# Performance work log

Measured on AMD Instinct MI355X. Metric: run time of the kernel, lower is better.

Reference implementation:

```python
import jax, jax.numpy as jnp
import numpy as np

B, S, D, H, FF = 4, 2048, 512, 8, 2048
HD = D // H
WINDOW = 64  # local attention half-window in rank space
EPS = 1e-5


def _layer_norm(v, g, b):
    m = jnp.mean(v, axis=-1, keepdims=True)
    var = jnp.mean(jnp.square(v - m), axis=-1, keepdims=True)
    return (v - m) / jnp.sqrt(var + EPS) * g + b


def setup_inputs() -> dict:
    key = jax.random.key(0)
    ks = jax.random.split(key, 10)
    sc = 0.02
    x = jax.random.normal(ks[0], (B, S, D), jnp.float32)
    padding_mask = jnp.zeros((B, S), dtype=bool)
    i = jnp.arange(S)
    local = jnp.abs(i[:, None] - i[None, :]) <= WINDOW
    glob = (i[:, None] == 0) | (i[None, :] == 0)  # global spectrum token at pos 0
    attn_mask = jnp.where(local | glob, 0.0, -jnp.inf).astype(jnp.float32)
    return {
        "x": x,
        "padding_mask": padding_mask,
        "attn_mask": attn_mask,
        "in_proj_w": jax.random.normal(ks[1], (3 * D, D), jnp.float32) * sc,
        "in_proj_b": jnp.zeros((3 * D,), jnp.float32),
        "out_proj_w": jax.random.normal(ks[2], (D, D), jnp.float32) * sc,
        "out_proj_b": jnp.zeros((D,), jnp.float32),
        "ln1_g": jnp.ones((D,), jnp.float32),
        "ln1_b": jnp.zeros((D,), jnp.float32),
        "ln2_g": jnp.ones((D,), jnp.float32),
        "ln2_b": jnp.zeros((D,), jnp.float32),
        "ff_w1": jax.random.normal(ks[3], (FF, D), jnp.float32) * sc,
        "ff_b1": jnp.zeros((FF,), jnp.float32),
        "ff_w2": jax.random.normal(ks[4], (D, FF), jnp.float32) * sc,
        "ff_b2": jnp.zeros((D,), jnp.float32),
    }


def reference(x, padding_mask, attn_mask, in_proj_w, in_proj_b, out_proj_w,
              out_proj_b, ln1_g, ln1_b, ln2_g, ln2_b, ff_w1, ff_b1, ff_w2, ff_b2):
    # pre-LN attention
    a = _layer_norm(x, ln1_g, ln1_b)
    qkv = a @ in_proj_w.T + in_proj_b  # [B,S,3D]
    q, k, v = jnp.split(qkv, 3, axis=-1)
    to_heads = lambda t: t.reshape(B, S, H, HD).transpose(0, 2, 1, 3)
    q, k, v = to_heads(q), to_heads(k), to_heads(v)
    scores = jnp.einsum('bhqd,bhkd->bhqk', q, k) * (HD ** -0.5)
    # float attn_mask path: key_padding_mask converted to additive -inf floats
    kpm = jnp.where(padding_mask, -jnp.inf, 0.0).astype(scores.dtype)
    scores = scores + attn_mask[None, None, :, :] + kpm[:, None, None, :]
    p = jax.nn.softmax(scores, axis=-1)
    o = jnp.einsum('bhqk,bhkd->bhqd', p, v).transpose(0, 2, 1, 3).reshape(B, S, D)
    o = o @ out_proj_w.T + out_proj_b
    x = x + o  # residual (dropout = 0)
    # pre-LN feed-forward with exact GELU (torch nn.GELU default)
    f = _layer_norm(x, ln2_g, ln2_b)
    f = jax.nn.gelu(f @ ff_w1.T + ff_b1, approximate=False) @ ff_w2.T + ff_b2
    return x + f
```

## Files before the change

### kernel.cpp

```cpp
#include <hip/hip_runtime.h>
#include <hip/hip_bf16.h>
#include <math.h>

namespace {

constexpr int kB = 4, kS = 2048, kD = 512, kH = 8, kFF = 2048;
constexpr int kM = kB * kS;
constexpr int kHD = kD / kH;
constexpr int kWin = 64;

typedef __attribute__((ext_vector_type(8))) short short8;
typedef __attribute__((ext_vector_type(4))) float f32x4;

__device__ __forceinline__ float bf2f(__hip_bfloat16 v) { return __bfloat162float(v); }
__device__ __forceinline__ __hip_bfloat16 f2bf(float v) { return __float2bfloat16(v); }
__device__ __forceinline__ int iclamp(int v, int lo, int hi) { return v < lo ? lo : (v > hi ? hi : v); }

__device__ __forceinline__ void async16(const void* g, void* l) {
  __builtin_amdgcn_global_load_lds((const __attribute__((address_space(1))) void*)g,
                                   (__attribute__((address_space(3))) void*)l, 16, 0, 0);
}

__global__ void cast_f32_bf16(const float* __restrict__ s, __hip_bfloat16* __restrict__ d, int n) {
  int i = (blockIdx.x * blockDim.x + threadIdx.x) * 4;
  if (i >= n) return;
  float4 v = *(const float4*)(s + i);
  union { __hip_bfloat16 h[4]; uint2 u; } t;
  t.h[0] = f2bf(v.x); t.h[1] = f2bf(v.y); t.h[2] = f2bf(v.z); t.h[3] = f2bf(v.w);
  *(uint2*)(d + i) = t.u;
}

__global__ __launch_bounds__(64)
void ln_rows(const float* __restrict__ x, const float* __restrict__ g,
             const float* __restrict__ bta, __hip_bfloat16* __restrict__ out) {
  int row = blockIdx.x;
  int lane = threadIdx.x;
  const float* xr = x + (size_t)row * kD;
  int c = lane * 8;
  float4 v0 = *(const float4*)(xr + c);
  float4 v1 = *(const float4*)(xr + c + 4);
  float s  = v0.x + v0.y + v0.z + v0.w + v1.x + v1.y + v1.z + v1.w;
  float ss = v0.x*v0.x + v0.y*v0.y + v0.z*v0.z + v0.w*v0.w
           + v1.x*v1.x + v1.y*v1.y + v1.z*v1.z + v1.w*v1.w;
#pragma unroll
  for (int o = 32; o > 0; o >>= 1) { s += __shfl_xor(s, o); ss += __shfl_xor(ss, o); }
  float mean = s * (1.0f / kD);
  float inv  = rsqrtf(ss * (1.0f / kD) - mean * mean + 1e-5f);
  float4 g0 = *(const float4*)(g + c),   g1 = *(const float4*)(g + c + 4);
  float4 b0 = *(const float4*)(bta + c), b1 = *(const float4*)(bta + c + 4);
  union { __hip_bfloat16 h[8]; int4 u; } t;
  t.h[0] = f2bf((v0.x - mean) * inv * g0.x + b0.x);
  t.h[1] = f2bf((v0.y - mean) * inv * g0.y + b0.y);
  t.h[2] = f2bf((v0.z - mean) * inv * g0.z + b0.z);
  t.h[3] = f2bf((v0.w - mean) * inv * g0.w + b0.w);
  t.h[4] = f2bf((v1.x - mean) * inv * g1.x + b1.x);
  t.h[5] = f2bf((v1.y - mean) * inv * g1.y + b1.y);
  t.h[6] = f2bf((v1.z - mean) * inv * g1.z + b1.z);
  t.h[7] = f2bf((v1.w - mean) * inv * g1.w + b1.w);
  *(int4*)(out + (size_t)row * kD + c) = t.u;
}

__global__ __launch_bounds__(64)
void transpose_v(const __hip_bfloat16* __restrict__ qkv, __hip_bfloat16* __restrict__ vt) {
  const int id = blockIdx.x;
  const int st = id & 31, h = (id >> 5) & 7, b = id >> 8;
  const int lane = threadIdx.x;
  __shared__ __hip_bfloat16 Ls[64 * 68];
  const int r8 = lane >> 3, c8 = (lane & 7) << 3;
  const __hip_bfloat16* src = qkv + (size_t)(b * kS + st * 64) * (3 * kD) + 2 * kD + h * kHD;
#pragma unroll
  for (int i = 0; i < 8; ++i) {
    int row = i * 8 + r8;
    union { int4 v; uint2 d2[2]; } u;
    u.v = *(const int4*)(src + (size_t)row * (3 * kD) + c8);
    *(uint2*)&Ls[row * 68 + c8] = u.d2[0];
    *(uint2*)&Ls[row * 68 + c8 + 4] = u.d2[1];
  }
  __syncthreads();
  __hip_bfloat16* dst = vt + (size_t)(b * kH + h) * kHD * kS + st * 64;
#pragma unroll
  for (int i = 0; i < 8; ++i) {
    int d = i * 8 + r8;
    union { __hip_bfloat16 hh[8]; int4 v; } u;
#pragma unroll
    for (int j = 0; j < 8; ++j) u.hh[j] = Ls[(c8 + j) * 68 + d];
    *(int4*)(dst + (size_t)d * kS + c8) = u.v;
  }
}

__global__ __launch_bounds__(64)
void attn_tile(const __hip_bfloat16* __restrict__ qkv, const __hip_bfloat16* __restrict__ vt,
               __hip_bfloat16* __restrict__ o) {
  const int bh = blockIdx.x;
  const int tq = blockIdx.y;
  const int b = bh >> 3, h = bh & 7;
  const int lane = threadIdx.x;
  const int quad = lane >> 4, col = lane & 15;
  const int q0 = tq * 16;
  const int kbase = q0 - kWin;

  __shared__ __hip_bfloat16 Pt[160 * 20];

  const __hip_bfloat16* base = qkv + (size_t)b * kS * (3 * kD);
  const __hip_bfloat16* vt_bh = vt + (size_t)(b * kH + h) * kHD * kS;

  short8 aq0, aq1;
  {
    const __hip_bfloat16* qrow = base + (size_t)(q0 + col) * (3 * kD) + h * kHD + quad * 8;
    aq0 = *(const short8*)qrow;
    aq1 = *(const short8*)(qrow + 32);
  }

  f32x4 sc[10];
#pragma unroll
  for (int t = 0; t < 10; ++t) {
    int krow = (t < 9) ? iclamp(kbase + t * 16 + col, 0, kS - 1) : col;
    const short8* kp = (const short8*)(base + (size_t)krow * (3 * kD) + kD + h * kHD + quad * 8);
    f32x4 a = (f32x4){0.f, 0.f, 0.f, 0.f};
    a = __builtin_amdgcn_mfma_f32_16x16x32_bf16(aq0, kp[0], a, 0, 0, 0);
    a = __builtin_amdgcn_mfma_f32_16x16x32_bf16(aq1, kp[4], a, 0, 0, 0);
    sc[t] = a;
  }

  float rowmax[4] = {-1e30f, -1e30f, -1e30f, -1e30f};
#pragma unroll
  for (int t = 0; t < 10; ++t) {
#pragma unroll
    for (int r = 0; r < 4; ++r) {
      int q = q0 + quad * 4 + r;
      bool valid;
      if (t < 9) {
        int k = kbase + t * 16 + col;
        valid = (k >= 0) && (k < kS) && ((q - k <= kWin && k - q <= kWin) || k == 0);
      } else {
        valid = (col == 0) && (kbase > 0);
      }
      float s = valid ? sc[t][r] * 0.125f : -1e30f;
      sc[t][r] = s;
      rowmax[r] = fmaxf(rowmax[r], s);
    }
  }
#pragma unroll
  for (int r = 0; r < 4; ++r)
#pragma unroll
    for (int off = 1; off < 16; off <<= 1)
      rowmax[r] = fmaxf(rowmax[r], __shfl_xor(rowmax[r], off));

  float rowsum[4] = {0.f, 0.f, 0.f, 0.f};
#pragma unroll
  for (int t = 0; t < 10; ++t)
#pragma unroll
    for (int r = 0; r < 4; ++r) {
      float e = __expf(sc[t][r] - rowmax[r]);
      sc[t][r] = e;
      rowsum[r] += e;
    }
#pragma unroll
  for (int r = 0; r < 4; ++r)
#pragma unroll
    for (int off = 1; off < 16; off <<= 1)
      rowsum[r] += __shfl_xor(rowsum[r], off);

#pragma unroll
  for (int t = 0; t < 10; ++t) {
    union { ushort u[4]; unsigned long long ll; } pk;
#pragma unroll
    for (int r = 0; r < 4; ++r) {
      __hip_bfloat16 hv = f2bf(sc[t][r]);
      pk.u[r] = *(ushort*)&hv;
    }
    *(unsigned long long*)&Pt[(t * 16 + col) * 20 + quad * 4] = pk.ll;
  }
  __syncthreads();

  f32x4 oacc[4];
#pragma unroll
  for (int n = 0; n < 4; ++n) oacc[n] = (f32x4){0.f, 0.f, 0.f, 0.f};

#pragma unroll
  for (int c = 0; c < 5; ++c) {
    union { short s[8]; short8 v; } pa;
#pragma unroll
    for (int j = 0; j < 8; ++j) pa.s[j] = *(const short*)&Pt[(c * 32 + quad * 8 + j) * 20 + col];
    const int kc = c * 32 + quad * 8;
    const int kstart = (kc < 144) ? iclamp(kbase + kc, 0, kS - 8) : (kc - 144);
#pragma unroll
    for (int n = 0; n < 4; ++n) {
      short8 vb = *(const short8*)(vt_bh + (size_t)(n * 16 + col) * kS + kstart);
      oacc[n] = __builtin_amdgcn_mfma_f32_16x16x32_bf16(pa.v, vb, oacc[n], 0, 0, 0);
    }
  }

#pragma unroll
  for (int n = 0; n < 4; ++n)
#pragma unroll
    for (int r = 0; r < 4; ++r) {
      int q = q0 + quad * 4 + r;
      o[(size_t)(b * kS + q) * kD + h * kHD + n * 16 + col] = f2bf(oacc[n][r] / rowsum[r]);
    }
}

__global__ __launch_bounds__(1024)
void attn_q0(const __hip_bfloat16* __restrict__ qkv, __hip_bfloat16* __restrict__ o) {
  const int b = blockIdx.x >> 3, h = blockIdx.x & 7;
  const int t = threadIdx.x;
  const int lane = t & 63, wid = t >> 6;
  __shared__ float qs[kHD];
  __shared__ float sc[kS];
  __shared__ float redm[16];
  __shared__ float reds[16];
  __shared__ float part[16][kHD];

  const __hip_bfloat16* base = qkv + (size_t)b * kS * (3 * kD);
  if (t < kHD) qs[t] = bf2f(base[h * kHD + t]) * 0.125f;
  __syncthreads();

  float m = -1e30f;
#pragma unroll
  for (int it = 0; it < 2; ++it) {
    int k = t + it * 1024;
    const short8* kp = (const short8*)(base + (size_t)k * (3 * kD) + kD + h * kHD);
    float s = 0.f;
#pragma unroll
    for (int cc = 0; cc < 8; ++cc) {
      union { short8 v; __hip_bfloat16 hh[8]; } u;
      u.v = kp[cc];
#pragma unroll
      for (int d = 0; d < 8; ++d) s += qs[cc * 8 + d] * bf2f(u.hh[d]);
    }
    sc[k] = s;
    m = fmaxf(m, s);
  }
#pragma unroll
  for (int off = 32; off > 0; off >>= 1) m = fmaxf(m, __shfl_xor(m, off));
  if (lane == 0) redm[wid] = m;
  __syncthreads();
  float M = redm[0];
#pragma unroll
  for (int i = 1; i < 16; ++i) M = fmaxf(M, redm[i]);

  float ls = 0.f;
#pragma unroll
  for (int it = 0; it < 2; ++it) {
    int k = t + it * 1024;
    float e = __expf(sc[k] - M);
    sc[k] = e;
    ls += e;
  }
#pragma unroll
  for (int off = 32; off > 0; off >>= 1) ls += __shfl_xor(ls, off);
  if (lane == 0) reds[wid] = ls;
  __syncthreads();
  float L = 0.f;
#pragma unroll
  for (int i = 0; i < 16; ++i) L += reds[i];

  float a = 0.f;
  const int d = lane;
#pragma unroll 8
  for (int kk = 0; kk < 128; ++kk) {
    int k = wid * 128 + kk;
    a += sc[k] * bf2f(base[(size_t)k * (3 * kD) + 2 * kD + h * kHD + d]);
  }
  part[wid][d] = a;
  __syncthreads();
  if (t < kHD) {
    float s = 0.f;
#pragma unroll
    for (int c = 0; c < 16; ++c) s += part[c][t];
    o[(size_t)(b * kS) * kD + h * kHD + t] = f2bf(s / L);
  }
}

template <int TN, int NB, int EPI, typename OT>
__global__ __launch_bounds__(256, (TN == 64) ? 4 : 3)
void gemm_bt(const __hip_bfloat16* __restrict__ A, const __hip_bfloat16* __restrict__ W,
             const float* __restrict__ bias, const float* __restrict__ resid,
             OT* __restrict__ C, int Ndim, int K) {
  constexpr int NF = TN / 32;
  __shared__ __hip_bfloat16 As[128 * 64];
  __shared__ __hip_bfloat16 Ws[TN * 64];

  const int id = blockIdx.x;
  const int rr = id & 7, tt = id >> 3;
  const int nb = tt % NB, mb = (tt / NB) * 8 + rr;

  const int tid = threadIdx.x;
  const int lane = tid & 63, w = tid >> 6;
  const int wm = w >> 1, wn = w & 1;
  const int quad = lane >> 4, mrow = lane & 15;
  const int m0 = mb * 128, n0 = nb * TN;

  const int lrow = lane >> 3;
  const int lcol = ((lane & 7) ^ lrow) << 3;

  f32x4 acc[4][NF];
#pragma unroll
  for (int i = 0; i < 4; ++i)
#pragma unroll
    for (int j = 0; j < NF; ++j) acc[i][j] = (f32x4){0.f, 0.f, 0.f, 0.f};

  for (int kt = 0; kt < K; kt += 64) {
#pragma unroll
    for (int it = 0; it < 4; ++it) {
      int c = w * 4 + it;
      async16(A + (size_t)(m0 + c * 8 + lrow) * K + kt + lcol, &As[c * 512]);
    }
#pragma unroll
    for (int it = 0; it < NF; ++it) {
      int c = w * NF + it;
      async16(W + (size_t)(n0 + c * 8 + lrow) * K + kt + lcol, &Ws[c * 512]);
    }
    __syncthreads();
#pragma unroll
    for (int kk = 0; kk < 64; kk += 32) {
      const int ch = (kk >> 3) + quad;
      const int sw = (ch ^ (mrow & 7)) << 3;
      short8 af[4], wf[NF];
#pragma unroll
      for (int i = 0; i < 4; ++i)
        af[i] = *(const short8*)&As[(wm * 64 + i * 16 + mrow) * 64 + sw];
#pragma unroll
      for (int j = 0; j < NF; ++j)
        wf[j] = *(const short8*)&Ws[(wn * (TN / 2) + j * 16 + mrow) * 64 + sw];
#pragma unroll
      for (int i = 0; i < 4; ++i)
#pragma unroll
        for (int j = 0; j < NF; ++j)
          acc[i][j] = __builtin_amdgcn_mfma_f32_16x16x32_bf16(af[i], wf[j], acc[i][j], 0, 0, 0);
    }
    __syncthreads();
  }

#pragma unroll
  for (int i = 0; i < 4; ++i) {
#pragma unroll
    for (int r = 0; r < 4; ++r) {
      int row = m0 + wm * 64 + i * 16 + quad * 4 + r;
#pragma unroll
      for (int j = 0; j < NF; ++j) {
        int col = n0 + wn * (TN / 2) + j * 16 + mrow;
        float v = acc[i][j][r] + bias[col];
        if (EPI == 1) v = 0.5f * v * (1.0f + erff(v * 0.70710678118f));
        if (EPI == 2) v += resid[(size_t)row * Ndim + col];
        if constexpr (__is_same(OT, float)) C[(size_t)row * Ndim + col] = v;
        else                                C[(size_t)row * Ndim + col] = f2bf(v);
      }
    }
  }
}

}

extern "C" void kernel_launch(void* const* d_in, const int* in_sizes, int n_in,
                              void* d_out, int out_size, void* d_ws, size_t ws_size,
                              hipStream_t stream) {
  const float* x          = (const float*)d_in[0];
  const float* in_proj_w  = (const float*)d_in[3];
  const float* in_proj_b  = (const float*)d_in[4];
  const float* out_proj_w = (const float*)d_in[5];
  const float* out_proj_b = (const float*)d_in[6];
  const float* ln1_g      = (const float*)d_in[7];
  const float* ln1_b      = (const float*)d_in[8];
  const float* ln2_g      = (const float*)d_in[9];
  const float* ln2_b      = (const float*)d_in[10];
  const float* ff_w1      = (const float*)d_in[11];
  const float* ff_b1      = (const float*)d_in[12];
  const float* ff_w2      = (const float*)d_in[13];
  const float* ff_b2      = (const float*)d_in[14];
  float* out = (float*)d_out;

  char* ws = (char*)d_ws;
  size_t off = 0;
  auto carve = [&](size_t bytes) { char* p = ws + off; off += (bytes + 255) & ~(size_t)255; return p; };
  __hip_bfloat16* wqkv_bf = (__hip_bfloat16*)carve((size_t)3 * kD * kD * 2);
  __hip_bfloat16* wout_bf = (__hip_bfloat16*)carve((size_t)kD * kD * 2);
  __hip_bfloat16* wff1_bf = (__hip_bfloat16*)carve((size_t)kFF * kD * 2);
  __hip_bfloat16* wff2_bf = (__hip_bfloat16*)carve((size_t)kD * kFF * 2);
  __hip_bfloat16* a_bf    = (__hip_bfloat16*)carve((size_t)kM * kD * 2);
  __hip_bfloat16* qkv_bf  = (__hip_bfloat16*)carve((size_t)kM * 3 * kD * 2);
  __hip_bfloat16* o_bf    = (__hip_bfloat16*)carve((size_t)kM * kD * 2);
  float*          r1      = (float*)carve((size_t)kM * kD * 4);
  __hip_bfloat16* ln2_bf  = (__hip_bfloat16*)carve((size_t)kM * kD * 2);
  __hip_bfloat16* ff1_bf  = (__hip_bfloat16*)carve((size_t)kM * kFF * 2);
  __hip_bfloat16* vt      = a_bf;

  {
    int n;
    n = 3 * kD * kD; cast_f32_bf16<<<(n / 4 + 255) / 256, 256, 0, stream>>>(in_proj_w, wqkv_bf, n);
    n = kD * kD;     cast_f32_bf16<<<(n / 4 + 255) / 256, 256, 0, stream>>>(out_proj_w, wout_bf, n);
    n = kFF * kD;    cast_f32_bf16<<<(n / 4 + 255) / 256, 256, 0, stream>>>(ff_w1, wff1_bf, n);
    n = kD * kFF;    cast_f32_bf16<<<(n / 4 + 255) / 256, 256, 0, stream>>>(ff_w2, wff2_bf, n);
  }

  ln_rows<<<kM, 64, 0, stream>>>(x, ln1_g, ln1_b, a_bf);
  gemm_bt<128, 12, 0, __hip_bfloat16><<<64 * 12, 256, 0, stream>>>(
      a_bf, wqkv_bf, in_proj_b, nullptr, qkv_bf, 3 * kD, kD);
  transpose_v<<<kB * kH * 32, 64, 0, stream>>>(qkv_bf, vt);
  attn_tile<<<dim3(kB * kH, kS / 16), 64, 0, stream>>>(qkv_bf, vt, o_bf);
  attn_q0<<<kB * kH, 1024, 0, stream>>>(qkv_bf, o_bf);
  gemm_bt<64, 8, 2, float><<<64 * 8, 256, 0, stream>>>(
      o_bf, wout_bf, out_proj_b, x, r1, kD, kD);
  ln_rows<<<kM, 64, 0, stream>>>(r1, ln2_g, ln2_b, ln2_bf);
  gemm_bt<128, 16, 1, __hip_bfloat16><<<64 * 16, 256, 0, stream>>>(
      ln2_bf, wff1_bf, ff_b1, nullptr, ff1_bf, kFF, kD);
  gemm_bt<64, 8, 2, float><<<64 * 8, 256, 0, stream>>>(
      ff1_bf, wff2_bf, ff_b2, r1, out, kD, kFF);
}
```

Baseline: 253.5 us.

## Fuse weight casts with LN1, write V transposed from QKV GEMM, store residual in bf16

Merges the four weight cast kernels and the first layer norm into one prep launch and packs four LN rows per block. The QKV GEMM epilogue now writes the V columns straight into the transposed layout, which removes the transpose kernel; attn_q0 reads V through that transposed buffer with vector loads. The intermediate residual r1 is stored in bf16 rather than fp32, halving its traffic but adding rounding error to the residual stream. The GEMM launch-bound occupancy hint for the TN=128 variant is raised from 3 to 4.

```diff
diff --git a/kernel.cpp b/kernel.cpp
--- a/kernel.cpp
+++ b/kernel.cpp
@@ -21,21 +21,8 @@
                                    (__attribute__((address_space(3))) void*)l, 16, 0, 0);
 }
 
-__global__ void cast_f32_bf16(const float* __restrict__ s, __hip_bfloat16* __restrict__ d, int n) {
-  int i = (blockIdx.x * blockDim.x + threadIdx.x) * 4;
-  if (i >= n) return;
-  float4 v = *(const float4*)(s + i);
-  union { __hip_bfloat16 h[4]; uint2 u; } t;
-  t.h[0] = f2bf(v.x); t.h[1] = f2bf(v.y); t.h[2] = f2bf(v.z); t.h[3] = f2bf(v.w);
-  *(uint2*)(d + i) = t.u;
-}
-
-__global__ __launch_bounds__(64)
-void ln_rows(const float* __restrict__ x, const float* __restrict__ g,
-             const float* __restrict__ bta, __hip_bfloat16* __restrict__ out) {
-  int row = blockIdx.x;
-  int lane = threadIdx.x;
-  const float* xr = x + (size_t)row * kD;
+__device__ __forceinline__ void ln_one_row_f32(const float* xr, const float* g,
+                                               const float* bta, __hip_bfloat16* outr, int lane) {
   int c = lane * 8;
   float4 v0 = *(const float4*)(xr + c);
   float4 v1 = *(const float4*)(xr + c + 4);
@@ -57,35 +44,62 @@
   t.h[5] = f2bf((v1.y - mean) * inv * g1.y + b1.y);
   t.h[6] = f2bf((v1.z - mean) * inv * g1.z + b1.z);
   t.h[7] = f2bf((v1.w - mean) * inv * g1.w + b1.w);
-  *(int4*)(out + (size_t)row * kD + c) = t.u;
-}
-
-__global__ __launch_bounds__(64)
-void transpose_v(const __hip_bfloat16* __restrict__ qkv, __hip_bfloat16* __restrict__ vt) {
+  *(int4*)(outr + c) = t.u;
+}
+
+__global__ __launch_bounds__(256)
+void prep(const float* __restrict__ iw, const float* __restrict__ ow,
+          const float* __restrict__ f1, const float* __restrict__ f2,
+          __hip_bfloat16* __restrict__ wq, __hip_bfloat16* __restrict__ wo,
+          __hip_bfloat16* __restrict__ w1, __hip_bfloat16* __restrict__ w2,
+          const float* __restrict__ x, const float* __restrict__ g,
+          const float* __restrict__ bta, __hip_bfloat16* __restrict__ a) {
   const int id = blockIdx.x;
-  const int st = id & 31, h = (id >> 5) & 7, b = id >> 8;
-  const int lane = threadIdx.x;
-  __shared__ __hip_bfloat16 Ls[64 * 68];
-  const int r8 = lane >> 3, c8 = (lane & 7) << 3;
-  const __hip_bfloat16* src = qkv + (size_t)(b * kS + st * 64) * (3 * kD) + 2 * kD + h * kHD;
-#pragma unroll
-  for (int i = 0; i < 8; ++i) {
-    int row = i * 8 + r8;
-    union { int4 v; uint2 d2[2]; } u;
-    u.v = *(const int4*)(src + (size_t)row * (3 * kD) + c8);
-    *(uint2*)&Ls[row * 68 + c8] = u.d2[0];
-    *(uint2*)&Ls[row * 68 + c8 + 4] = u.d2[1];
-  }
-  __syncthreads();
-  __hip_bfloat16* dst = vt + (size_t)(b * kH + h) * kHD * kS + st * 64;
-#pragma unroll
-  for (int i = 0; i < 8; ++i) {
-    int d = i * 8 + r8;
-    union { __hip_bfloat16 hh[8]; int4 v; } u;
-#pragma unroll
-    for (int j = 0; j < 8; ++j) u.hh[j] = Ls[(c8 + j) * 68 + d];
-    *(int4*)(dst + (size_t)d * kS + c8) = u.v;
-  }
+  if (id < 3072) {
+    const float* s; __hip_bfloat16* d; int base;
+    if (id < 768)       { s = iw; d = wq; base = id; }
+    else if (id < 1024) { s = ow; d = wo; base = id - 768; }
+    else if (id < 2048) { s = f1; d = w1; base = id - 1024; }
+    else                { s = f2; d = w2; base = id - 2048; }
+    int i = base * 1024 + threadIdx.x * 4;
+    float4 v = *(const float4*)(s + i);
+    union { __hip_bfloat16 h[4]; uint2 u; } t;
+    t.h[0] = f2bf(v.x); t.h[1] = f2bf(v.y); t.h[2] = f2bf(v.z); t.h[3] = f2bf(v.w);
+    *(uint2*)(d + i) = t.u;
+  } else {
+    int row = (id - 3072) * 4 + (threadIdx.x >> 6);
+    ln_one_row_f32(x + (size_t)row * kD, g, bta, a + (size_t)row * kD, threadIdx.x & 63);
+  }
+}
+
+__global__ __launch_bounds__(256)
+void ln_rows_bf(const __hip_bfloat16* __restrict__ x, const float* __restrict__ g,
+                const float* __restrict__ bta, __hip_bfloat16* __restrict__ out) {
+  int row = blockIdx.x * 4 + (threadIdx.x >> 6);
+  int lane = threadIdx.x & 63;
+  int c = lane * 8;
+  union { short8 v; __hip_bfloat16 hh[8]; } u;
+  u.v = *(const short8*)(x + (size_t)row * kD + c);
+  float f[8];
+  float s = 0.f, ss = 0.f;
+#pragma unroll
+  for (int i = 0; i < 8; ++i) { f[i] = bf2f(u.hh[i]); s += f[i]; ss += f[i] * f[i]; }
+#pragma unroll
+  for (int o = 32; o > 0; o >>= 1) { s += __shfl_xor(s, o); ss += __shfl_xor(ss, o); }
+  float mean = s * (1.0f / kD);
+  float inv  = rsqrtf(ss * (1.0f / kD) - mean * mean + 1e-5f);
+  float4 g0 = *(const float4*)(g + c),   g1 = *(const float4*)(g + c + 4);
+  float4 b0 = *(const float4*)(bta + c), b1 = *(const float4*)(bta + c + 4);
+  union { __hip_bfloat16 h[8]; int4 v; } t;
+  t.h[0] = f2bf((f[0] - mean) * inv * g0.x + b0.x);
+  t.h[1] = f2bf((f[1] - mean) * inv * g0.y + b0.y);
+  t.h[2] = f2bf((f[2] - mean) * inv * g0.z + b0.z);
+  t.h[3] = f2bf((f[3] - mean) * inv * g0.w + b0.w);
+  t.h[4] = f2bf((f[4] - mean) * inv * g1.x + b1.x);
+  t.h[5] = f2bf((f[5] - mean) * inv * g1.y + b1.y);
+  t.h[6] = f2bf((f[6] - mean) * inv * g1.z + b1.z);
+  t.h[7] = f2bf((f[7] - mean) * inv * g1.w + b1.w);
+  *(int4*)(out + (size_t)row * kD + c) = t.v;
 }
 
 __global__ __launch_bounds__(64)
@@ -201,7 +215,8 @@
 }
 
 __global__ __launch_bounds__(1024)
-void attn_q0(const __hip_bfloat16* __restrict__ qkv, __hip_bfloat16* __restrict__ o) {
+void attn_q0(const __hip_bfloat16* __restrict__ qkv, const __hip_bfloat16* __restrict__ vt,
+             __hip_bfloat16* __restrict__ o) {
   const int b = blockIdx.x >> 3, h = blockIdx.x & 7;
   const int t = threadIdx.x;
   const int lane = t & 63, wid = t >> 6;
@@ -212,6 +227,7 @@
   __shared__ float part[16][kHD];
 
   const __hip_bfloat16* base = qkv + (size_t)b * kS * (3 * kD);
+  const __hip_bfloat16* vt_bh = vt + (size_t)(b * kH + h) * kHD * kS;
   if (t < kHD) qs[t] = bf2f(base[h * kHD + t]) * 0.125f;
   __syncthreads();
 
@@ -257,10 +273,13 @@
 
   float a = 0.f;
   const int d = lane;
-#pragma unroll 8
-  for (int kk = 0; kk < 128; ++kk) {
-    int k = wid * 128 + kk;
-    a += sc[k] * bf2f(base[(size_t)k * (3 * kD) + 2 * kD + h * kHD + d]);
+  const __hip_bfloat16* vr = vt_bh + (size_t)d * kS + wid * 128;
+#pragma unroll
+  for (int c = 0; c < 16; ++c) {
+    union { short8 v; __hip_bfloat16 hh[8]; } u;
+    u.v = *(const short8*)(vr + c * 8);
+#pragma unroll
+    for (int j = 0; j < 8; ++j) a += sc[wid * 128 + c * 8 + j] * bf2f(u.hh[j]);
   }
   part[wid][d] = a;
   __syncthreads();
@@ -272,11 +291,11 @@
   }
 }
 
-template <int TN, int NB, int EPI, typename OT>
-__global__ __launch_bounds__(256, (TN == 64) ? 4 : 3)
+template <int TN, int NB, int EPI, int WVT, typename OT, typename RT>
+__global__ __launch_bounds__(256, (TN == 64) ? 4 : 4)
 void gemm_bt(const __hip_bfloat16* __restrict__ A, const __hip_bfloat16* __restrict__ W,
-             const float* __restrict__ bias, const float* __restrict__ resid,
-             OT* __restrict__ C, int Ndim, int K) {
+             const float* __restrict__ bias, const RT* __restrict__ resid,
+             OT* __restrict__ C, __hip_bfloat16* __restrict__ vt, int Ndim, int K) {
   constexpr int NF = TN / 32;
   __shared__ __hip_bfloat16 As[128 * 64];
   __shared__ __hip_bfloat16 Ws[TN * 64];
@@ -332,6 +351,25 @@
     __syncthreads();
   }
 
+  if (WVT && n0 >= 1024) {
+#pragma unroll
+    for (int i = 0; i < 4; ++i) {
+      int row0 = m0 + wm * 64 + i * 16 + quad * 4;
+      int bb = row0 >> 11, ss = row0 & 2047;
+#pragma unroll
+      for (int j = 0; j < NF; ++j) {
+        int colv = n0 + wn * (TN / 2) + j * 16 + mrow - 1024;
+        int hh = colv >> 6, dd = colv & 63;
+        float bsv = bias[1024 + colv];
+        union { __hip_bfloat16 h[4]; unsigned long long u; } pk;
+#pragma unroll
+        for (int r = 0; r < 4; ++r) pk.h[r] = f2bf(acc[i][j][r] + bsv);
+        *(unsigned long long*)(vt + ((size_t)(bb * kH + hh) * kHD + dd) * kS + ss) = pk.u;
+      }
+    }
+    return;
+  }
+
 #pragma unroll
   for (int i = 0; i < 4; ++i) {
 #pragma unroll
@@ -342,7 +380,8 @@
         int col = n0 + wn * (TN / 2) + j * 16 + mrow;
         float v = acc[i][j][r] + bias[col];
         if (EPI == 1) v = 0.5f * v * (1.0f + erff(v * 0.70710678118f));
-        if (EPI == 2) v += resid[(size_t)row * Ndim + col];
+        if (EPI == 2) v += ((const float*)resid)[(size_t)row * Ndim + col];
+        if (EPI == 3) v += bf2f(((const __hip_bfloat16*)resid)[(size_t)row * Ndim + col]);
         if constexpr (__is_same(OT, float)) C[(size_t)row * Ndim + col] = v;
         else                                C[(size_t)row * Ndim + col] = f2bf(v);
       }
@@ -379,31 +418,24 @@
   __hip_bfloat16* wff2_bf = (__hip_bfloat16*)carve((size_t)kD * kFF * 2);
   __hip_bfloat16* a_bf    = (__hip_bfloat16*)carve((size_t)kM * kD * 2);
   __hip_bfloat16* qkv_bf  = (__hip_bfloat16*)carve((size_t)kM * 3 * kD * 2);
+  __hip_bfloat16* vt      = (__hip_bfloat16*)carve((size_t)kM * kD * 2);
   __hip_bfloat16* o_bf    = (__hip_bfloat16*)carve((size_t)kM * kD * 2);
-  float*          r1      = (float*)carve((size_t)kM * kD * 4);
+  __hip_bfloat16* r1b     = (__hip_bfloat16*)carve((size_t)kM * kD * 2);
   __hip_bfloat16* ln2_bf  = (__hip_bfloat16*)carve((size_t)kM * kD * 2);
   __hip_bfloat16* ff1_bf  = (__hip_bfloat16*)carve((size_t)kM * kFF * 2);
-  __hip_bfloat16* vt      = a_bf;
-
-  {
-    int n;
-    n = 3 * kD * kD; cast_f32_bf16<<<(n / 4 + 255) / 256, 256, 0, stream>>>(in_proj_w, wqkv_bf, n);
-    n = kD * kD;     cast_f32_bf16<<<(n / 4 + 255) / 256, 256, 0, stream>>>(out_proj_w, wout_bf, n);
-    n = kFF * kD;    cast_f32_bf16<<<(n / 4 + 255) / 256, 256, 0, stream>>>(ff_w1, wff1_bf, n);
-    n = kD * kFF;    cast_f32_bf16<<<(n / 4 + 255) / 256, 256, 0, stream>>>(ff_w2, wff2_bf, n);
-  }
-
-  ln_rows<<<kM, 64, 0, stream>>>(x, ln1_g, ln1_b, a_bf);
-  gemm_bt<128, 12, 0, __hip_bfloat16><<<64 * 12, 256, 0, stream>>>(
-      a_bf, wqkv_bf, in_proj_b, nullptr, qkv_bf, 3 * kD, kD);
-  transpose_v<<<kB * kH * 32, 64, 0, stream>>>(qkv_bf, vt);
+
+  prep<<<5120, 256, 0, stream>>>(in_proj_w, out_proj_w, ff_w1, ff_w2,
+                                 wqkv_bf, wout_bf, wff1_bf, wff2_bf,
+                                 x, ln1_g, ln1_b, a_bf);
+  gemm_bt<128, 12, 0, 1, __hip_bfloat16, float><<<64 * 12, 256, 0, stream>>>(
+      a_bf, wqkv_bf, in_proj_b, nullptr, qkv_bf, vt, 3 * kD, kD);
   attn_tile<<<dim3(kB * kH, kS / 16), 64, 0, stream>>>(qkv_bf, vt, o_bf);
-  attn_q0<<<kB * kH, 1024, 0, stream>>>(qkv_bf, o_bf);
-  gemm_bt<64, 8, 2, float><<<64 * 8, 256, 0, stream>>>(
-      o_bf, wout_bf, out_proj_b, x, r1, kD, kD);
-  ln_rows<<<kM, 64, 0, stream>>>(r1, ln2_g, ln2_b, ln2_bf);
-  gemm_bt<128, 16, 1, __hip_bfloat16><<<64 * 16, 256, 0, stream>>>(
-      ln2_bf, wff1_bf, ff_b1, nullptr, ff1_bf, kFF, kD);
-  gemm_bt<64, 8, 2, float><<<64 * 8, 256, 0, stream>>>(
-      ff1_bf, wff2_bf, ff_b2, r1, out, kD, kFF);
-}
+  attn_q0<<<kB * kH, 1024, 0, stream>>>(qkv_bf, vt, o_bf);
+  gemm_bt<64, 8, 2, 0, __hip_bfloat16, float><<<64 * 8, 256, 0, stream>>>(
+      o_bf, wout_bf, out_proj_b, x, r1b, nullptr, kD, kD);
+  ln_rows_bf<<<kM / 4, 256, 0, stream>>>(r1b, ln2_g, ln2_b, ln2_bf);
+  gemm_bt<128, 16, 1, 0, __hip_bfloat16, float><<<64 * 16, 256, 0, stream>>>(
+      ln2_bf, wff1_bf, ff_b1, nullptr, ff1_bf, nullptr, kFF, kD);
+  gemm_bt<64, 8, 3, 0, float, __hip_bfloat16><<<64 * 8, 256, 0, stream>>>(
+      ff1_bf, wff2_bf, ff_b2, r1b, out, nullptr, kD, kFF);
+}
```

Measured after the change: 250.5 us. No clear change (-1.2%).
